# Optimization experiments

Hardware: AMD Instinct MI355X
Metric: run time of the kernel (lower is better)

Reference implementation:

```python
import jax, jax.numpy as jnp
import numpy as np

HORIZON = 24   # forecast horizon (<= M)
M = 24         # seasonality period
B = 16384      # batch_size
T = 2048       # time_steps


def setup_inputs() -> dict:
    key = jax.random.key(0)
    kx, = jax.random.split(key, 1)
    x = jax.random.uniform(kx, (B, T, 1), dtype=jnp.float32, minval=0.1, maxval=1.0)
    # learned parameters of the ES layer
    alpha = jnp.array([0.3], dtype=jnp.float32)
    gamma = jnp.array([0.3], dtype=jnp.float32)
    init_seasonality = jnp.full((M,), 0.8, dtype=jnp.float32)
    level = jnp.array([0.8], dtype=jnp.float32)
    return {"x": x, "alpha": alpha, "gamma": gamma,
            "init_seasonality": init_seasonality, "level": level}


def _es_forward(x, alpha, gamma, init_seasonality, level):
    Bx, Tx = x.shape[0], x.shape[1]
    a = alpha[0]
    g = gamma[0]
    # Fuse batch into one long series: first example's full window, then the
    # last timestep of each subsequent example (stride-1 sliding windows).
    ts = jnp.concatenate([x[0, :, 0], x[1:, Tx - 1, 0]])  # (B+T-1,)

    def step(carry, y_t):
        l_prev, q = carry                     # q: (M,) seasonality circular buffer
        s_t = q[0]                            # deque.popleft()
        l_t = a * y_t / s_t + (1.0 - a) * l_prev
        s_new = g * y_t / l_t + (1.0 - g) * s_t
        q2 = jnp.concatenate([q[1:], s_new[None]])  # deque.append(s_new)
        xn = y_t / (s_t * l_t)
        return (l_t, q2), (xn, l_t, q2[:HORIZON])

    _, (xns, lts, qheads) = jax.lax.scan(step, (level[0], init_seasonality), ts)
    # Per-example denorm coefficients: recorded for steps i >= T-1.
    lev = lts[Tx - 1:]                        # (B,)
    seas = qheads[Tx - 1:]                    # (B, HORIZON)
    denorm = jnp.stack(
        [jnp.broadcast_to(lev[:, None], (Bx, HORIZON)), seas], axis=-1)  # (B,H,2)
    # Sliding windows of the normalized series: x_out[i] = xns[i:i+T]
    idx = jnp.arange(Bx)[:, None] + jnp.arange(Tx)[None, :]  # (B,T)
    x_out = xns[idx][..., None]               # (B,T,1)
    return x_out, denorm


def reference(x, alpha, gamma, init_seasonality, level):
    return _es_forward(x, alpha, gamma, init_seasonality, level)
```

## Files before the change

### kernel.cpp

```cpp
#include <hip/hip_runtime.h>

#define TT 2048
#define BB 16384
#define NSTEP 18431
#define HOR 24
#define MM 24

#define PCH 64
#define CLEN 288
#define WARM 1440

#define SEG 20480

#define FILLA_BLOCKS 32768
#define FILLB_BLOCKS 1536

__device__ __forceinline__ float frcp(float x) {
    float r = __builtin_amdgcn_rcpf(x);
    return r * fmaf(-x, r, 2.0f);
}
__device__ __forceinline__ float frcp_fast(float x) {
    return __builtin_amdgcn_rcpf(x);
}

__global__ void __launch_bounds__(256) prep_kernel(const float* __restrict__ x,
                                                   const float* __restrict__ init_seas,
                                                   float* __restrict__ ws) {
    int tid = blockIdx.x * blockDim.x + threadIdx.x;
    float* ts   = ws;
    float* Sarr = ws + 3 * SEG;
    if (tid < SEG) {
        float v;
        if (tid < TT)          v = x[tid];
        else if (tid < NSTEP)  v = x[(size_t)(tid - (TT - 1)) * TT + (TT - 1)];
        else                   v = 1.0f;
        ts[tid] = v;
    }
    if (tid < MM) Sarr[tid] = init_seas[tid];
}

__global__ void __launch_bounds__(64, 1) scan_kernel(const float* __restrict__ alpha,
                                                     const float* __restrict__ gamma,
                                                     const float* __restrict__ init_seas,
                                                     const float* __restrict__ level,
                                                     float* __restrict__ ws) {
    const int i = threadIdx.x;
    const float* ts = ws;
    float* xn    = ws + SEG;
    float* larr  = ws + 2 * SEG;
    float* Sarr  = ws + 3 * SEG;
    float* mwarm = ws + 4 * SEG;
    float* mend  = ws + 4 * SEG + PCH;

    const float a  = alpha[0];
    const float g  = gamma[0];
    const float oa = 1.0f - a;
    const float og = 1.0f - g;

    float l = level[0];
    float s[MM];
#pragma unroll
    for (int j = 0; j < MM; ++j) s[j] = init_seas[j];

    const int cstart = i * CLEN;
    int t = cstart - WARM;
    if (t < 0) t = 0;

    for (; t < cstart; t += MM) {
        float yv[MM];
#pragma unroll
        for (int q = 0; q < MM / 4; ++q) {
            const float4 v = *(const float4*)(ts + t + 4 * q);
            yv[4*q+0] = v.x; yv[4*q+1] = v.y; yv[4*q+2] = v.z; yv[4*q+3] = v.w;
        }
#pragma unroll
        for (int j = 0; j < MM; ++j) {
            const float y  = yv[j];
            const float u  = y * frcp_fast(s[j]);
            l = fmaf(oa, l, a * u);
            s[j] = fmaf(og, s[j], g * y * frcp_fast(l));
        }
    }
    {
        float m = 0.0f;
#pragma unroll
        for (int j = 0; j < MM; ++j) m += __log2f(s[j]);
        mwarm[i] = m;
    }

    const int cend = cstart + CLEN;
    for (; t < cend; t += MM) {
        float yv[MM], xv[MM], lv[MM], sv[MM];
#pragma unroll
        for (int q = 0; q < MM / 4; ++q) {
            const float4 v = *(const float4*)(ts + t + 4 * q);
            yv[4*q+0] = v.x; yv[4*q+1] = v.y; yv[4*q+2] = v.z; yv[4*q+3] = v.w;
        }
#pragma unroll
        for (int j = 0; j < MM; ++j) {
            const float y  = yv[j];
            const float u  = y * frcp(s[j]);
            l = fmaf(oa, l, a * u);
            const float rl = frcp(l);
            s[j] = fmaf(og, s[j], g * y * rl);
            xv[j] = u * rl;
            lv[j] = l;
            sv[j] = s[j];
        }
#pragma unroll
        for (int q = 0; q < MM / 4; ++q) {
            *(float4*)(xn   + t + 4 * q)      = make_float4(xv[4*q], xv[4*q+1], xv[4*q+2], xv[4*q+3]);
            *(float4*)(larr + t + 4 * q)      = make_float4(lv[4*q], lv[4*q+1], lv[4*q+2], lv[4*q+3]);
            *(float4*)(Sarr + MM + t + 4 * q) = make_float4(sv[4*q], sv[4*q+1], sv[4*q+2], sv[4*q+3]);
        }
    }
    {
        float m = 0.0f;
#pragma unroll
        for (int j = 0; j < MM; ++j) m += __log2f(s[j]);
        mend[i] = m;
    }
}

__global__ void __launch_bounds__(256) fix_kernel(float* __restrict__ ws) {
    float* larr  = ws + 2 * SEG;
    float* Sarr  = ws + 3 * SEG;
    float* mwarm = ws + 4 * SEG;
    float* mend  = ws + 4 * SEG + PCH;
    __shared__ float lam[PCH], ilam[PCH];

    if (threadIdx.x == 0) {
        float ll = 0.0f;
        lam[0] = 1.0f; ilam[0] = 1.0f;
        for (int c = 1; c < PCH; ++c) {
            ll += (mend[c - 1] - mwarm[c]) * (1.0f / 24.0f);
            lam[c]  = exp2f(ll);
            ilam[c] = exp2f(-ll);
        }
    }
    __syncthreads();

    const int NT = PCH * CLEN;
    for (int t = threadIdx.x; t < NT; t += blockDim.x)
        larr[t] *= ilam[t / CLEN];
    for (int t = threadIdx.x; t < NT; t += blockDim.x)
        Sarr[MM + t] *= lam[t / CLEN];
}

__global__ void __launch_bounds__(256) fill_kernel(const float* __restrict__ ws,
                                                   float* __restrict__ out) {
    const float* xn   = ws + SEG;
    const float* larr = ws + 2 * SEG;
    const float* Sarr = ws + 3 * SEG;
    const int bid = blockIdx.x;

    if (bid < FILLA_BLOCKS) {
        const int q  = bid * 256 + threadIdx.x;
        const int b  = q >> 9;
        const int t0 = (q & 511) << 2;
        const int src = b + t0;
        const float4 v = make_float4(xn[src], xn[src + 1], xn[src + 2], xn[src + 3]);
        *(float4*)(out + ((size_t)b * TT + t0)) = v;
    } else {
        const int r = (bid - FILLA_BLOCKS) * 256 + threadIdx.x;
        const int b = r / HOR;
        const int h = r - b * HOR;
        const float lev = larr[(TT - 1) + b];
        const float se  = Sarr[TT + b + h];
        *(float2*)(out + (size_t)BB * TT + 2 * (size_t)r) = make_float2(lev, se);
    }
}

extern "C" void kernel_launch(void* const* d_in, const int* in_sizes, int n_in,
                              void* d_out, int out_size, void* d_ws, size_t ws_size,
                              hipStream_t stream) {
    const float* x     = (const float*)d_in[0];
    const float* alpha = (const float*)d_in[1];
    const float* gamma = (const float*)d_in[2];
    const float* iseas = (const float*)d_in[3];
    const float* level = (const float*)d_in[4];
    float* ws  = (float*)d_ws;
    float* out = (float*)d_out;

    prep_kernel<<<SEG / 256, 256, 0, stream>>>(x, iseas, ws);
    scan_kernel<<<1, PCH, 0, stream>>>(alpha, gamma, iseas, level, ws);
    fix_kernel<<<1, 256, 0, stream>>>(ws);
    fill_kernel<<<FILLA_BLOCKS + FILLB_BLOCKS, 256, 0, stream>>>(ws, out);
}
```

Baseline: 288.9 us.

## Double scan chunks, fold correction prefix into scan, apply scale in fill

The serial ES scan now runs on 128 chunks of length 144 with a shorter warmup, so each thread's dependent chain is shorter. The per-chunk log-scale correction is computed with an in-block parallel prefix sum at the end of the scan kernel, and the separate fix kernel is removed. The chunk scale factors are instead applied lazily in the fill kernel when reading level and seasonality. The fill kernel's main output is written with nontemporal stores. Together these cut one launch and the serial scan latency, at the risk of lower accuracy from the shorter warmup.

```diff
diff --git a/kernel.cpp b/kernel.cpp
--- a/kernel.cpp
+++ b/kernel.cpp
@@ -6,14 +6,16 @@
 #define HOR 24
 #define MM 24
 
-#define PCH 64
-#define CLEN 288
-#define WARM 1440
+#define PCH 128
+#define CLEN 144
+#define WARM 1248
 
 #define SEG 20480
 
 #define FILLA_BLOCKS 32768
 #define FILLB_BLOCKS 1536
+
+typedef float f4v __attribute__((ext_vector_type(4)));
 
 __device__ __forceinline__ float frcp(float x) {
     float r = __builtin_amdgcn_rcpf(x);
@@ -39,18 +41,20 @@
     if (tid < MM) Sarr[tid] = init_seas[tid];
 }
 
-__global__ void __launch_bounds__(64, 1) scan_kernel(const float* __restrict__ alpha,
-                                                     const float* __restrict__ gamma,
-                                                     const float* __restrict__ init_seas,
-                                                     const float* __restrict__ level,
-                                                     float* __restrict__ ws) {
+__global__ void __launch_bounds__(PCH, 1) scan_kernel(const float* __restrict__ alpha,
+                                                      const float* __restrict__ gamma,
+                                                      const float* __restrict__ init_seas,
+                                                      const float* __restrict__ level,
+                                                      float* __restrict__ ws) {
     const int i = threadIdx.x;
     const float* ts = ws;
     float* xn    = ws + SEG;
     float* larr  = ws + 2 * SEG;
     float* Sarr  = ws + 3 * SEG;
-    float* mwarm = ws + 4 * SEG;
-    float* mend  = ws + 4 * SEG + PCH;
+    float* lamg  = ws + 4 * SEG;
+    float* ilamg = ws + 4 * SEG + PCH;
+
+    __shared__ float sm_warm[PCH], sm_end[PCH], sm_ll[PCH];
 
     const float a  = alpha[0];
     const float g  = gamma[0];
@@ -85,7 +89,7 @@
         float m = 0.0f;
 #pragma unroll
         for (int j = 0; j < MM; ++j) m += __log2f(s[j]);
-        mwarm[i] = m;
+        sm_warm[i] = m;
     }
 
     const int cend = cstart + CLEN;
@@ -118,40 +122,32 @@
         float m = 0.0f;
 #pragma unroll
         for (int j = 0; j < MM; ++j) m += __log2f(s[j]);
-        mend[i] = m;
-    }
-}
-
-__global__ void __launch_bounds__(256) fix_kernel(float* __restrict__ ws) {
-    float* larr  = ws + 2 * SEG;
-    float* Sarr  = ws + 3 * SEG;
-    float* mwarm = ws + 4 * SEG;
-    float* mend  = ws + 4 * SEG + PCH;
-    __shared__ float lam[PCH], ilam[PCH];
-
-    if (threadIdx.x == 0) {
-        float ll = 0.0f;
-        lam[0] = 1.0f; ilam[0] = 1.0f;
-        for (int c = 1; c < PCH; ++c) {
-            ll += (mend[c - 1] - mwarm[c]) * (1.0f / 24.0f);
-            lam[c]  = exp2f(ll);
-            ilam[c] = exp2f(-ll);
-        }
+        sm_end[i] = m;
     }
     __syncthreads();
 
-    const int NT = PCH * CLEN;
-    for (int t = threadIdx.x; t < NT; t += blockDim.x)
-        larr[t] *= ilam[t / CLEN];
-    for (int t = threadIdx.x; t < NT; t += blockDim.x)
-        Sarr[MM + t] *= lam[t / CLEN];
+    float d = (i == 0) ? 0.0f : (sm_end[i - 1] - sm_warm[i]) * (1.0f / 24.0f);
+    sm_ll[i] = d;
+    __syncthreads();
+#pragma unroll
+    for (int off = 1; off < PCH; off <<= 1) {
+        float add = (i >= off) ? sm_ll[i - off] : 0.0f;
+        __syncthreads();
+        sm_ll[i] += add;
+        __syncthreads();
+    }
+    const float ll = sm_ll[i];
+    lamg[i]  = exp2f(ll);
+    ilamg[i] = exp2f(-ll);
 }
 
 __global__ void __launch_bounds__(256) fill_kernel(const float* __restrict__ ws,
                                                    float* __restrict__ out) {
-    const float* xn   = ws + SEG;
-    const float* larr = ws + 2 * SEG;
-    const float* Sarr = ws + 3 * SEG;
+    const float* xn    = ws + SEG;
+    const float* larr  = ws + 2 * SEG;
+    const float* Sarr  = ws + 3 * SEG;
+    const float* lamg  = ws + 4 * SEG;
+    const float* ilamg = ws + 4 * SEG + PCH;
     const int bid = blockIdx.x;
 
     if (bid < FILLA_BLOCKS) {
@@ -159,14 +155,23 @@
         const int b  = q >> 9;
         const int t0 = (q & 511) << 2;
         const int src = b + t0;
-        const float4 v = make_float4(xn[src], xn[src + 1], xn[src + 2], xn[src + 3]);
-        *(float4*)(out + ((size_t)b * TT + t0)) = v;
+        f4v v;
+        v.x = xn[src]; v.y = xn[src + 1]; v.z = xn[src + 2]; v.w = xn[src + 3];
+        __builtin_nontemporal_store(v, (f4v*)(out + ((size_t)b * TT + t0)));
     } else {
+        __shared__ float slam[PCH], silam[PCH];
+        if (threadIdx.x < PCH) {
+            slam[threadIdx.x]  = lamg[threadIdx.x];
+            silam[threadIdx.x] = ilamg[threadIdx.x];
+        }
+        __syncthreads();
         const int r = (bid - FILLA_BLOCKS) * 256 + threadIdx.x;
         const int b = r / HOR;
         const int h = r - b * HOR;
-        const float lev = larr[(TT - 1) + b];
-        const float se  = Sarr[TT + b + h];
+        const int tl = (TT - 1) + b;
+        const int tsx = TT + b + h;
+        const float lev = larr[tl]  * silam[tl / CLEN];
+        const float se  = Sarr[tsx] * slam[(tsx - MM) / CLEN];
         *(float2*)(out + (size_t)BB * TT + 2 * (size_t)r) = make_float2(lev, se);
     }
 }
@@ -184,6 +189,5 @@
 
     prep_kernel<<<SEG / 256, 256, 0, stream>>>(x, iseas, ws);
     scan_kernel<<<1, PCH, 0, stream>>>(alpha, gamma, iseas, level, ws);
-    fix_kernel<<<1, 256, 0, stream>>>(ws);
     fill_kernel<<<FILLA_BLOCKS + FILLB_BLOCKS, 256, 0, stream>>>(ws, out);
 }
```

New measurement: 248.9 us. 1.16x faster.
